# Optimization experiments

Hardware: AMD Instinct MI355X
Metric: run time of the kernel (lower is better)

The kernel has to match this reference:

```python
import jax, jax.numpy as jnp
import numpy as np
from jax import lax

B, CIN, HC, D, H, W = 4, 16, 16, 31, 128, 128


def setup_inputs() -> dict:
    key = jax.random.key(0)
    k1, k2, k3, k4, k5 = jax.random.split(key, 5)
    inputs = jax.random.normal(k1, (B, CIN, D, H, W), dtype=jnp.float32)
    # Conv3d weight: [out=2*HC, in=CIN, 3,3,3]
    conv_w = jax.random.normal(k2, (2 * HC, CIN, 3, 3, 3), dtype=jnp.float32) * 0.05
    # FFN weights stored as [in, out] (equivalent to torch Linear weight.T)
    w1 = jax.random.normal(k3, (HC, 2 * HC), dtype=jnp.float32) * 0.1
    w2 = jax.random.normal(k4, (2 * HC, HC), dtype=jnp.float32) * 0.1
    w3 = jax.random.normal(k5, (HC, 2 * HC), dtype=jnp.float32) * 0.1
    return {"inputs": inputs, "conv_w": conv_w, "w1": w1, "w2": w2, "w3": w3,
            "reverse": 0}


def reference(inputs, conv_w, w1, w2, w3, reverse):
    hc = conv_w.shape[0] // 2
    # 3D conv producing 2*hc gate channels  [B, 2hc, D, H, W]
    gates = lax.conv_general_dilated(
        inputs, conv_w, window_strides=(1, 1, 1), padding='SAME',
        dimension_numbers=('NCDHW', 'OIDHW', 'NCDHW'))
    Z = jnp.tanh(gates[:, :hc])            # [B, hc, D, H, W]
    F = jax.nn.sigmoid(gates[:, hc:])
    # scan over depth (spectral) dim; h0 = 0 reproduces h = (1-f)*z at step 0
    Zs = jnp.moveaxis(Z, 2, 0)             # [D, B, hc, H, W]
    Fs = jnp.moveaxis(F, 2, 0)
    if reverse:
        Zs, Fs = Zs[::-1], Fs[::-1]

    def step(h, zf):
        z, f = zf
        h = f * h + (1.0 - f) * z
        return h, h

    h0 = jnp.zeros_like(Zs[0])
    _, hs = lax.scan(step, h0, (Zs, Fs))   # [D, B, hc, H, W]
    if reverse:
        hs = hs[::-1]
    out = jnp.moveaxis(hs, 0, 2)           # [B, hc, D, H, W]
    # channel-enhanced FFN on channel-last layout
    x = jnp.moveaxis(out, 1, -1)           # [B, D, H, W, hc]
    x1 = jnp.dot(jax.nn.gelu(jnp.dot(x, w1), approximate=False), w2)
    g = jnp.dot(x, w3)                     # [B, D, H, W, 2hc]
    a, wg = jnp.split(g, 2, axis=-1)
    y = x1 + a * jax.nn.sigmoid(wg)
    return jnp.moveaxis(y, -1, 1)          # [B, hc, D, H, W]
```

## Files before the change

kernel.cpp:

```cpp
#include <hip/hip_runtime.h>
#include <hip/hip_fp16.h>

#define HC 16
#define CIN 16
#define BD 31
#define HH 128
#define WW 128
#define PLANE (HH*WW)
#define CH_STRIDE (BD*PLANE)

typedef __attribute__((ext_vector_type(8))) short bf16x8;
typedef __attribute__((ext_vector_type(16))) float f32x16;

__device__ __forceinline__ float sigmoid_fast(float x) {
    return __builtin_amdgcn_rcpf(1.0f + __expf(-x));
}
__device__ __forceinline__ float tanh_fast(float x) {
    return fmaf(2.0f, __builtin_amdgcn_rcpf(1.0f + __expf(-2.0f * x)), -1.0f);
}
__device__ __forceinline__ ushort f2bf(float f) {
    unsigned u = __float_as_uint(f);
    u = (u + 0x7fffu + ((u >> 16) & 1u)) >> 16;
    return (ushort)u;
}
__device__ __forceinline__ unsigned pack_bf2(float lo, float hi) {
    unsigned r;
    asm("v_cvt_pk_bf16_f32 %0, %1, %2" : "=v"(r) : "v"(lo), "v"(hi));
    return r;
}
__device__ __forceinline__ float gelu_as(float s) {
    float z  = 0.70710678118f * s;
    float az = fabsf(z);
    float t  = __builtin_amdgcn_rcpf(fmaf(0.3275911f, az, 1.0f));
    float p  = t * (0.254829592f + t * (-0.284496736f + t * (1.421413741f
             + t * (-1.453152027f + t * 1.061405429f))));
    float e  = __expf(-z * z);
    float er = copysignf(1.0f - p * e, z);
    return 0.5f * s * (1.0f + er);
}

__global__ __launch_bounds__(256)
void xprep_kernel(const float* __restrict__ inp, char* __restrict__ xT,
                  const float* __restrict__ cw,
                  const float* __restrict__ w1,
                  const float* __restrict__ w2,
                  const float* __restrict__ w3,
                  ushort* __restrict__ wtab, ushort* __restrict__ wtab2)
{
    if (blockIdx.x >= 7936) {
        int idx = (blockIdx.x - 7936) * 256 + threadIdx.x;
        if (idx < 13824) {
            int j    = idx & 7;
            int lane = (idx >> 3) & 63;
            int t    = (idx >> 9) % 9;
            int kd   = (idx >> 9) / 9;
            int co = lane & 31;
            int ci = 8 * (lane >> 5) + j;
            int kh = t / 3, kw = t % 3;
            wtab[idx] = f2bf(cw[(co * CIN + ci) * 27 + kd * 9 + kh * 3 + kw]);
            return;
        }
        idx -= 13824;
        if (idx >= 2048) return;
        int e    = idx & 7;
        int lane = (idx >> 3) & 63;
        int tbl  = idx >> 9;
        int m  = lane & 31;
        int hi = lane >> 5;
        int k  = (e & 3) + 8 * (e >> 2) + 4 * hi;
        float v = 0.f;
        if (tbl == 0)      v = w1[k * 32 + m];
        else if (tbl == 3) v = w3[k * 32 + m];
        else {
            int mf = tbl - 1;
            if (m < 16) v = w2[(k + 16 * mf) * 16 + m];
        }
        wtab2[idx] = f2bf(v);
        return;
    }

    __shared__ float tile[16][256];
    int t  = threadIdx.x;
    int hp = blockIdx.x & 63;
    int g  = blockIdx.x >> 6;
    int d  = g % BD;
    int b  = g / BD;

    size_t src = (size_t)b * CIN * CH_STRIDE + (size_t)d * PLANE + hp * 256;
    #pragma unroll
    for (int c = 0; c < 16; ++c)
        tile[c][t] = inp[src + (size_t)c * CH_STRIDE + t];
    __syncthreads();

    int w  = t & 127;
    int rr = t >> 7;
    char* rowp = xT + (((size_t)(b * BD + d) * 128) + hp * 2 + rr) * 4096;
    #pragma unroll
    for (int q = 0; q < 2; ++q) {
        uint4 pk;
        pk.x = (unsigned)f2bf(tile[q*8+0][t]) | ((unsigned)f2bf(tile[q*8+1][t]) << 16);
        pk.y = (unsigned)f2bf(tile[q*8+2][t]) | ((unsigned)f2bf(tile[q*8+3][t]) << 16);
        pk.z = (unsigned)f2bf(tile[q*8+4][t]) | ((unsigned)f2bf(tile[q*8+5][t]) << 16);
        pk.w = (unsigned)f2bf(tile[q*8+6][t]) | ((unsigned)f2bf(tile[q*8+7][t]) << 16);
        unsigned off = ((unsigned)((w + 1) * 32 + q * 16) ^ (((unsigned)(w + 1) & 0xE) << 3)) - 32;
        *(uint4*)(rowp + off) = pk;
    }
}

#define SLOT_B (3 * 4224)

__device__ __forceinline__ void gload_lds16(const void* g, void* l) {
    __builtin_amdgcn_global_load_lds(
        (const __attribute__((address_space(1))) unsigned int*)g,
        (__attribute__((address_space(3))) unsigned int*)l, 16, 0, 0);
}

__global__ __launch_bounds__(256, 2)
void qrnn_convscan(const char* __restrict__ xT,
                   const ushort* __restrict__ wtab,
                   char* __restrict__ hbuf,
                   const int* __restrict__ rev_p)
{
    __shared__ __align__(16) char slab[4][SLOT_B];

    int p = blockIdx.x;
    int logical = (p & 7) * 64 + (p >> 3);
    int b  = logical >> 7;
    int ht = logical & 127;
    int rev = rev_p[0];

    int lane = threadIdx.x & 63;
    int wid  = threadIdx.x >> 6;
    int wl   = lane & 31;
    int hi   = lane >> 5;
    int cio  = hi * 16;

    const bf16x8* wt = (const bf16x8*)wtab;
    bf16x8 af[27];
    #pragma unroll
    for (int t = 0; t < 27; ++t) af[t] = wt[t * 64 + lane];

    unsigned bpo[3];
    #pragma unroll
    for (int dwn = 0; dwn < 3; ++dwn) {
        unsigned wc = (unsigned)(wl + dwn);
        bpo[dwn] = (unsigned)(wid * 1024) + ((wc * 32 + cio) ^ ((wc & 0xE) << 3));
    }

    for (int i = threadIdx.x; i < 4 * 3 * 32; i += 256) {
        int s = i / 96;
        int r = (i / 32) % 3;
        int k = i & 31;
        int off = (k < 8) ? (k * 4) : (4128 + (k - 8) * 4);
        *(int*)(slab[s] + r * 4224 + off) = 0;
    }

    auto zero_slot = [&](int s) {
        for (int i = threadIdx.x; i < 768; i += 256) {
            int r = i >> 8;
            int k = i & 255;
            *(uint4*)(slab[s] + r * 4224 + 32 + k * 16) = uint4{0, 0, 0, 0};
        }
    };

    auto stage = [&](int s, int plane) {
        const char* pl = xT + ((size_t)(b * BD + plane) * 128) * 4096;
        for (int c = wid; c < 12; c += 4) {
            int rr = c >> 2, ch = c & 3;
            int h = ht - 1 + rr;
            char* dst = slab[s] + rr * 4224 + 32 + ch * 1024;
            if ((unsigned)h < (unsigned)HH)
                gload_lds16(pl + (size_t)h * 4096 + ch * 1024 + lane * 16, dst);
            else
                *(uint4*)(dst + lane * 16) = uint4{0, 0, 0, 0};
        }
    };

    f32x16 zacc;
    #pragma unroll
    for (int r = 0; r < 16; ++r) zacc[r] = 0.f;

    auto convd = [&](int d) -> f32x16 {
        f32x16 A = zacc;
        #pragma unroll
        for (int kd = 0; kd < 3; ++kd) {
            const char* sb = slab[(d - 1 + kd) & 3];
            #pragma unroll
            for (int t = 0; t < 9; ++t) {
                bf16x8 bfr = *(const bf16x8*)(sb + (t / 3) * 4224 + bpo[t % 3]);
                A = __builtin_amdgcn_mfma_f32_32x32x16_bf16(af[kd * 9 + t], bfr, A, 0, 0, 0);
            }
        }
        return A;
    };

    float h[8];
    #pragma unroll
    for (int j = 0; j < 8; ++j) h[j] = 0.f;

    int pix = ht * WW + wid * 32 + wl;
    char* hb0 = hbuf + ((size_t)b * BD * PLANE + pix) * 32 + hi * 16;

    auto tail = [&](const f32x16& A, int d) {
        union { uint4 u4; unsigned u[4]; } bx;
        #pragma unroll
        for (int r = 0; r < 8; ++r) {
            float z = tanh_fast(A[r]);
            float f = sigmoid_fast(A[r + 8]);
            h[r] = z + f * (h[r] - z);
        }
        #pragma unroll
        for (int q = 0; q < 4; ++q)
            bx.u[q] = pack_bf2(h[2 * q], h[2 * q + 1]);
        *(uint4*)(hb0 + (size_t)d * (PLANE * 32)) = bx.u4;
    };

    int d0  = rev ? (BD - 1) : 0;
    int sgn = rev ? -1 : 1;
    int oobq = rev ? -1 : BD;

    stage(d0 & 3, d0);
    stage((d0 + sgn) & 3, d0 + sgn);
    zero_slot((d0 - sgn) & 3);
    __syncthreads();

    f32x16 accP;
    {
        int q = d0 + 2 * sgn;
        if (q >= 0 && q < BD) stage(q & 3, q);
        accP = convd(d0);
        __syncthreads();
    }

    #pragma unroll 1
    for (int i = 1; i < BD; ++i) {
        int d = d0 + sgn * i;
        int q = d + 2 * sgn;
        if (q >= 0 && q < BD) stage(q & 3, q);
        else if (q == oobq)   zero_slot(q & 3);

        f32x16 acc = convd(d);
        tail(accP, d - sgn);
        accP = acc;

        __syncthreads();
    }
    tail(accP, d0 + sgn * (BD - 1));
}

__global__ __launch_bounds__(256)
void mlp_mfma_kernel(const char* __restrict__ hbuf,
                     const ushort* __restrict__ wtab2,
                     float* __restrict__ out)
{
    int lane = threadIdx.x & 63;
    int wid  = threadIdx.x >> 6;
    int p    = lane & 31;
    int hi   = lane >> 5;

    size_t tile = (size_t)blockIdx.x * 4 + wid;
    size_t ptg  = tile * 32 + p;

    const bf16x8* W = (const bf16x8*)wtab2;
    bf16x8 af1  = W[lane];
    bf16x8 af2a = W[64 + lane];
    bf16x8 af2b = W[128 + lane];
    bf16x8 af3  = W[192 + lane];
    bf16x8 bx   = *(const bf16x8*)(hbuf + ptg * 32 + hi * 16);

    f32x16 zacc;
    #pragma unroll
    for (int r = 0; r < 16; ++r) zacc[r] = 0.f;

    f32x16 a1 = __builtin_amdgcn_mfma_f32_32x32x16_bf16(af1, bx, zacc, 0, 0, 0);
    f32x16 a3 = __builtin_amdgcn_mfma_f32_32x32x16_bf16(af3, bx, zacc, 0, 0, 0);

    union { bf16x8 v; unsigned u[4]; } b2a, b2b;
    #pragma unroll
    for (int q = 0; q < 4; ++q) {
        b2a.u[q] = pack_bf2(gelu_as(a1[2 * q]),     gelu_as(a1[2 * q + 1]));
        b2b.u[q] = pack_bf2(gelu_as(a1[8 + 2 * q]), gelu_as(a1[8 + 2 * q + 1]));
    }

    f32x16 a2 = __builtin_amdgcn_mfma_f32_32x32x16_bf16(af2a, b2a.v, zacc, 0, 0, 0);
    a2 = __builtin_amdgcn_mfma_f32_32x32x16_bf16(af2b, b2b.v, a2, 0, 0, 0);

    int bd  = (int)(ptg >> 14);
    int pix = (int)(ptg & 16383);
    int b   = bd / BD;
    int d   = bd % BD;
    float* obase = out + (size_t)b * HC * CH_STRIDE + (size_t)d * PLANE + pix;

    #pragma unroll
    for (int r = 0; r < 8; ++r) {
        int c = (r & 3) + 8 * (r >> 2) + 4 * hi;
        float y = a2[r] + a3[r] * sigmoid_fast(a3[r + 8]);
        obase[(size_t)c * CH_STRIDE] = y;
    }
}

extern "C" void kernel_launch(void* const* d_in, const int* in_sizes, int n_in,
                              void* d_out, int out_size, void* d_ws, size_t ws_size,
                              hipStream_t stream)
{
    const float* inp = (const float*)d_in[0];
    const float* cw  = (const float*)d_in[1];
    const float* w1  = (const float*)d_in[2];
    const float* w2  = (const float*)d_in[3];
    const float* w3  = (const float*)d_in[4];
    const int*   rev = (const int*)d_in[5];

    ushort* wtab  = (ushort*)d_ws;
    ushort* wtab2 = (ushort*)((char*)d_ws + 27648);
    char*   xT    = (char*)d_ws + 32768;
    char*   hbuf  = (char*)d_ws + 32768 + (size_t)4 * BD * 128 * 4096;

    xprep_kernel<<<dim3(7998), dim3(256), 0, stream>>>(
        inp, xT, cw, w1, w2, w3, wtab, wtab2);

    qrnn_convscan<<<dim3(512), dim3(256), 0, stream>>>(
        xT, wtab, hbuf, rev);

    mlp_mfma_kernel<<<dim3(15872), dim3(256), 0, stream>>>(
        hbuf, wtab2, (float*)d_out);
}
```

Measured before the change: 149.3 us.

## Reuse each staged depth plane across three rotating accumulators in conv-scan

Restructures the depth loop so that each input plane is read from LDS once and fed into three accumulators, one per kd tap, which rotate roles every step. Before, each output depth re-read three planes. This cuts LDS B-fragment reads per output by about a factor of three and drops zero_slot, since the boundary planes are simply never accumulated. In exchange it holds three 16-float accumulators live, which raises VGPR/AGPR pressure, and the 3-way manual unroll adds control flow.

```diff
diff --git a/kernel.cpp b/kernel.cpp
--- a/kernel.cpp
+++ b/kernel.cpp
@@ -128,6 +128,8 @@
     int b  = logical >> 7;
     int ht = logical & 127;
     int rev = rev_p[0];
+    int sgn = rev ? -1 : 1;
+    int d0  = rev ? (BD - 1) : 0;
 
     int lane = threadIdx.x & 63;
     int wid  = threadIdx.x >> 6;
@@ -136,9 +138,15 @@
     int cio  = hi * 16;
 
     const bf16x8* wt = (const bf16x8*)wtab;
-    bf16x8 af[27];
-    #pragma unroll
-    for (int t = 0; t < 27; ++t) af[t] = wt[t * 64 + lane];
+    int kdA = rev ? 0 : 2;
+    int kdC = rev ? 2 : 0;
+    bf16x8 afA[9], afB[9], afC[9];
+    #pragma unroll
+    for (int t = 0; t < 9; ++t) {
+        afA[t] = wt[(kdA * 9 + t) * 64 + lane];
+        afB[t] = wt[(9      + t) * 64 + lane];
+        afC[t] = wt[(kdC * 9 + t) * 64 + lane];
+    }
 
     unsigned bpo[3];
     #pragma unroll
@@ -155,20 +163,13 @@
         *(int*)(slab[s] + r * 4224 + off) = 0;
     }
 
-    auto zero_slot = [&](int s) {
-        for (int i = threadIdx.x; i < 768; i += 256) {
-            int r = i >> 8;
-            int k = i & 255;
-            *(uint4*)(slab[s] + r * 4224 + 32 + k * 16) = uint4{0, 0, 0, 0};
-        }
-    };
-
-    auto stage = [&](int s, int plane) {
+    auto stage = [&](int plane) {
         const char* pl = xT + ((size_t)(b * BD + plane) * 128) * 4096;
+        char* sb = slab[plane & 3];
         for (int c = wid; c < 12; c += 4) {
             int rr = c >> 2, ch = c & 3;
             int h = ht - 1 + rr;
-            char* dst = slab[s] + rr * 4224 + 32 + ch * 1024;
+            char* dst = sb + rr * 4224 + 32 + ch * 1024;
             if ((unsigned)h < (unsigned)HH)
                 gload_lds16(pl + (size_t)h * 4096 + ch * 1024 + lane * 16, dst);
             else
@@ -179,20 +180,6 @@
     f32x16 zacc;
     #pragma unroll
     for (int r = 0; r < 16; ++r) zacc[r] = 0.f;
-
-    auto convd = [&](int d) -> f32x16 {
-        f32x16 A = zacc;
-        #pragma unroll
-        for (int kd = 0; kd < 3; ++kd) {
-            const char* sb = slab[(d - 1 + kd) & 3];
-            #pragma unroll
-            for (int t = 0; t < 9; ++t) {
-                bf16x8 bfr = *(const bf16x8*)(sb + (t / 3) * 4224 + bpo[t % 3]);
-                A = __builtin_amdgcn_mfma_f32_32x32x16_bf16(af[kd * 9 + t], bfr, A, 0, 0, 0);
-            }
-        }
-        return A;
-    };
 
     float h[8];
     #pragma unroll
@@ -215,37 +202,36 @@
         *(uint4*)(hb0 + (size_t)d * (PLANE * 32)) = bx.u4;
     };
 
-    int d0  = rev ? (BD - 1) : 0;
-    int sgn = rev ? -1 : 1;
-    int oobq = rev ? -1 : BD;
-
-    stage(d0 & 3, d0);
-    stage((d0 + sgn) & 3, d0 + sgn);
-    zero_slot((d0 - sgn) & 3);
+    auto step = [&](int i, f32x16& X, f32x16& Y, f32x16& Z) {
+        if (i > BD) return;
+        int q = d0 + sgn * i;
+        if (i + 2 < BD) stage(d0 + sgn * (i + 2));
+        if (i < BD) {
+            const char* sb = slab[q & 3];
+            #pragma unroll
+            for (int t = 0; t < 9; ++t) {
+                bf16x8 B = *(const bf16x8*)(sb + (t / 3) * 4224 + bpo[t % 3]);
+                X = __builtin_amdgcn_mfma_f32_32x32x16_bf16(afA[t], B, X, 0, 0, 0);
+                Y = __builtin_amdgcn_mfma_f32_32x32x16_bf16(afB[t], B, Y, 0, 0, 0);
+                Z = __builtin_amdgcn_mfma_f32_32x32x16_bf16(afC[t], B, Z, 0, 0, 0);
+            }
+        }
+        if (i >= 1) tail(X, q - sgn);
+        X = zacc;
+        __syncthreads();
+    };
+
+    stage(d0);
+    stage(d0 + sgn);
     __syncthreads();
 
-    f32x16 accP;
-    {
-        int q = d0 + 2 * sgn;
-        if (q >= 0 && q < BD) stage(q & 3, q);
-        accP = convd(d0);
-        __syncthreads();
-    }
-
+    f32x16 accA = zacc, accB = zacc, accC = zacc;
     #pragma unroll 1
-    for (int i = 1; i < BD; ++i) {
-        int d = d0 + sgn * i;
-        int q = d + 2 * sgn;
-        if (q >= 0 && q < BD) stage(q & 3, q);
-        else if (q == oobq)   zero_slot(q & 3);
-
-        f32x16 acc = convd(d);
-        tail(accP, d - sgn);
-        accP = acc;
-
-        __syncthreads();
-    }
-    tail(accP, d0 + sgn * (BD - 1));
+    for (int i = 0; i <= BD; i += 3) {
+        step(i,     accA, accB, accC);
+        step(i + 1, accB, accC, accA);
+        step(i + 2, accC, accA, accB);
+    }
 }
 
 __global__ __launch_bounds__(256)
```

Result: no change. 148.6 us (-0.5%).
